# Kernel optimization log

Measured on AMD Instinct MI355X. Metric: run time of the kernel, lower is better.

The kernel has to match this reference:

```python
import jax, jax.numpy as jnp
import numpy as np

D_MODEL = 1024
NUM_HEADS = 16
D_K = D_MODEL // NUM_HEADS


def setup_inputs() -> dict:
    key = jax.random.key(0)
    ks = jax.random.split(key, 12)
    B, S = 2, 2048
    s = 1.0 / np.sqrt(D_MODEL)
    inp = {
        "query": jax.random.normal(ks[0], (B, S, D_MODEL), jnp.float32),
        "key": jax.random.normal(ks[1], (B, S, D_MODEL), jnp.float32),
        "value": jax.random.normal(ks[2], (B, S, D_MODEL), jnp.float32),
        "Wq": jax.random.normal(ks[3], (D_MODEL, D_MODEL), jnp.float32) * s,
        "bq": jax.random.normal(ks[4], (D_MODEL,), jnp.float32) * s,
        "Wk": jax.random.normal(ks[5], (D_MODEL, D_MODEL), jnp.float32) * s,
        "bk": jax.random.normal(ks[6], (D_MODEL,), jnp.float32) * s,
        "Wv": jax.random.normal(ks[7], (D_MODEL, D_MODEL), jnp.float32) * s,
        "bv": jax.random.normal(ks[8], (D_MODEL,), jnp.float32) * s,
        "Wo": jax.random.normal(ks[9], (D_MODEL, D_MODEL), jnp.float32) * s,
        "bo": jax.random.normal(ks[10], (D_MODEL,), jnp.float32) * s,
    }
    return inp


def _split_heads(x):
    B, S, _ = x.shape
    return x.reshape(B, S, NUM_HEADS, D_K).transpose(0, 2, 1, 3)  # [B,H,S,Dk]


def reference(query, key, value, Wq, bq, Wk, bk, Wv, bv, Wo, bo):
    # Linear projections (torch Linear: x @ W.T + b)
    Q = _split_heads(query @ Wq.T + bq)
    K = _split_heads(key @ Wk.T + bk)
    V = _split_heads(value @ Wv.T + bv)
    scale = 1.0 / jnp.sqrt(jnp.asarray(D_K, Q.dtype))
    scores = jnp.einsum('bhqd,bhkd->bhqk', Q, K) * scale  # [B,H,S,S]
    attn = jax.nn.softmax(scores, axis=-1)
    # dropout is identity in eval mode
    x = jnp.einsum('bhqk,bhkd->bhqd', attn, V)
    B, H, S, Dk = x.shape
    x = x.transpose(0, 2, 1, 3).reshape(B, S, H * Dk)
    return x @ Wo.T + bo
```

## Files before the change

kernel.cpp:

```cpp
#include <hip/hip_runtime.h>
#include <hip/hip_bf16.h>

typedef __bf16 bf16;
typedef __attribute__((ext_vector_type(4))) __bf16 bf16x4;
typedef __attribute__((ext_vector_type(8))) __bf16 bf16x8;
typedef __attribute__((ext_vector_type(4))) float f32x4;
typedef __attribute__((ext_vector_type(16))) float f32x16;
typedef unsigned int u32;

#define D_MODEL 1024
#define NHEADS 16
#define DK 64
#define BATCH 2
#define SEQ 2048
#define NTOK (BATCH * SEQ)

#define QSCALE 0.18033688011112042f
#define DEFER_THR 8.0f

__device__ __forceinline__ u32 cvtpk_bf16(float lo, float hi) {
  u32 r;
  asm("v_cvt_pk_bf16_f32 %0, %1, %2" : "=v"(r) : "v"(lo), "v"(hi));
  return r;
}
__device__ __forceinline__ void plswap(u32& a, u32& b) {
  asm("v_permlane32_swap_b32 %0, %1" : "+v"(a), "+v"(b));
}
__device__ __forceinline__ float fast_exp2(float x) {
#if __has_builtin(__builtin_amdgcn_exp2f)
  return __builtin_amdgcn_exp2f(x);
#else
  return exp2f(x);
#endif
}
__device__ __forceinline__ float xhalf_max(float x) {
  return fmaxf(x, __shfl_xor(x, 32));
}
__device__ __forceinline__ float xhalf_add(float x) {
  return x + __shfl_xor(x, 32);
}

__device__ __forceinline__ int frag_off_q(int s, int d) {
  return ((s >> 5) << 11) + ((d >> 4) << 9) + ((((d >> 3) & 1) * 32 + (s & 31)) << 3) + (d & 7);
}
__device__ __forceinline__ int frag_off_k(int s, int d) {
  return ((s >> 6) << 12) + ((((s >> 5) & 1) * 4 + (d >> 4)) << 9) +
         ((((d >> 3) & 1) * 32 + (s & 31)) << 3) + (d & 7);
}
__device__ __forceinline__ int frag_off_v(int s, int d) {
  return ((s >> 6) << 12) + (((d >> 5) * 4 + ((s >> 4) & 3)) << 9) +
         ((((s >> 3) & 1) * 32 + (d & 31)) << 3) + (s & 7);
}

__global__ __launch_bounds__(256) void cvt3_kernel(
    const float* __restrict__ s0, const float* __restrict__ s1, const float* __restrict__ s2,
    bf16* __restrict__ d0, bf16* __restrict__ d1, bf16* __restrict__ d2, int n4) {
  int i = blockIdx.x * blockDim.x + threadIdx.x;
  if (i >= n4) return;
  const float* s = blockIdx.y == 0 ? s0 : blockIdx.y == 1 ? s1 : s2;
  bf16* d = blockIdx.y == 0 ? d0 : blockIdx.y == 1 ? d1 : d2;
  float4 v = reinterpret_cast<const float4*>(s)[i];
  bf16x4 o;
  o[0] = (bf16)v.x; o[1] = (bf16)v.y; o[2] = (bf16)v.z; o[3] = (bf16)v.w;
  reinterpret_cast<bf16x4*>(d)[i] = o;
}

__global__ __launch_bounds__(256) void cvt4_kernel(
    const float* __restrict__ s0, const float* __restrict__ s1,
    const float* __restrict__ s2, const float* __restrict__ s3,
    bf16* __restrict__ d0, bf16* __restrict__ d1, bf16* __restrict__ d2, bf16* __restrict__ d3,
    int n4) {
  int i = blockIdx.x * blockDim.x + threadIdx.x;
  if (i >= n4) return;
  const float* s = blockIdx.y == 0 ? s0 : blockIdx.y == 1 ? s1 : blockIdx.y == 2 ? s2 : s3;
  bf16* d = blockIdx.y == 0 ? d0 : blockIdx.y == 1 ? d1 : blockIdx.y == 2 ? d2 : d3;
  float4 v = reinterpret_cast<const float4*>(s)[i];
  bf16x4 o;
  o[0] = (bf16)v.x; o[1] = (bf16)v.y; o[2] = (bf16)v.z; o[3] = (bf16)v.w;
  reinterpret_cast<bf16x4*>(d)[i] = o;
}

#define ASYNC_COPY16(gptr, lptr)                                                \
  __builtin_amdgcn_global_load_lds(                                             \
      (__attribute__((address_space(1))) void*)(gptr),                          \
      (__attribute__((address_space(3))) void*)(lptr), 16, 0, 0)

struct ProjArgs {
  const bf16* A[3];
  const bf16* W[3];
  const float* bias[3];
  bf16* out[3];
};

__global__ __launch_bounds__(256) void gemm_proj(ProjArgs pa, int K) {
  __shared__ bf16 As[128][32];
  __shared__ bf16 Bs[128][32];
  const int z = blockIdx.z;
  const bf16* A = pa.A[z];
  const bf16* Bw = pa.W[z];
  const int m0 = blockIdx.x * 128;
  const int n0 = blockIdx.y * 128;

  const int t = threadIdx.x;
  const int wave = t >> 6;
  const int lane = t & 63;
  const int wr = (wave >> 1) * 64;
  const int wc = (wave & 1) * 64;
  const int r4 = lane >> 2;
  const int c8 = (lane & 3) * 8;
  const int fr = lane & 15;
  const int fk = (lane >> 4) * 8;

  f32x4 acc[4][4] = {};

  for (int k0 = 0; k0 < K; k0 += 32) {
    ASYNC_COPY16(&A[(size_t)(m0 + wave * 16 + r4) * K + k0 + c8], &As[wave * 16][0]);
    ASYNC_COPY16(&A[(size_t)(m0 + 64 + wave * 16 + r4) * K + k0 + c8], &As[64 + wave * 16][0]);
    ASYNC_COPY16(&Bw[(size_t)(n0 + wave * 16 + r4) * K + k0 + c8], &Bs[wave * 16][0]);
    ASYNC_COPY16(&Bw[(size_t)(n0 + 64 + wave * 16 + r4) * K + k0 + c8], &Bs[64 + wave * 16][0]);
    __syncthreads();

    bf16x8 af[4], bfr[4];
#pragma unroll
    for (int m = 0; m < 4; m++)
      af[m] = *reinterpret_cast<const bf16x8*>(&As[wr + m * 16 + fr][fk]);
#pragma unroll
    for (int n = 0; n < 4; n++)
      bfr[n] = *reinterpret_cast<const bf16x8*>(&Bs[wc + n * 16 + fr][fk]);
#pragma unroll
    for (int m = 0; m < 4; m++)
#pragma unroll
      for (int n = 0; n < 4; n++)
        acc[m][n] = __builtin_amdgcn_mfma_f32_16x16x32_bf16(af[m], bfr[n], acc[m][n], 0, 0, 0);
    __syncthreads();
  }

  const float scale = (z == 0) ? QSCALE : 1.0f;
  const float* bias = pa.bias[z];
  bf16* out = pa.out[z];
#pragma unroll
  for (int m = 0; m < 4; m++) {
#pragma unroll
    for (int n = 0; n < 4; n++) {
      const int col = n0 + wc + n * 16 + fr;
      const float bv = bias[col];
#pragma unroll
      for (int j = 0; j < 4; j++) {
        const int row = m0 + wr + m * 16 + (lane >> 4) * 4 + j;
        const float v = (acc[m][n][j] + bv) * scale;
        const int b = row >> 11;
        const int s = row & (SEQ - 1);
        const int h = col >> 6;
        const int d = col & (DK - 1);
        const size_t base = (size_t)(b * NHEADS + h) * SEQ * DK;
        int off;
        if (z == 0)      off = frag_off_q(s, d);
        else if (z == 1) off = frag_off_k(s, d);
        else             off = frag_off_v(s, d);
        out[base + off] = (bf16)v;
      }
    }
  }
}

#define TM 128
#define TN 64
#define BK 32

__global__ __launch_bounds__(256) void gemm_out(
    const bf16* __restrict__ A, const bf16* __restrict__ Bw,
    const float* __restrict__ bias, float* __restrict__ out, int K) {
  __shared__ bf16 As[TM][BK];
  __shared__ bf16 Bs[TN][BK];
  const int m0 = blockIdx.x * TM;
  const int n0 = blockIdx.y * TN;

  const int t = threadIdx.x;
  const int wave = t >> 6;
  const int lane = t & 63;
  const int wr = (wave >> 1) * 64;
  const int wc = (wave & 1) * 32;
  const int r4 = lane >> 2;
  const int c8 = (lane & 3) * 8;
  const int fr = lane & 15;
  const int fk = (lane >> 4) * 8;

  f32x4 acc[4][2] = {};
  for (int k0 = 0; k0 < K; k0 += BK) {
    ASYNC_COPY16(&A[(size_t)(m0 + wave * 16 + r4) * K + k0 + c8], &As[wave * 16][0]);
    ASYNC_COPY16(&A[(size_t)(m0 + 64 + wave * 16 + r4) * K + k0 + c8], &As[64 + wave * 16][0]);
    ASYNC_COPY16(&Bw[(size_t)(n0 + wave * 16 + r4) * K + k0 + c8], &Bs[wave * 16][0]);
    __syncthreads();

    bf16x8 af[4], bfr[2];
#pragma unroll
    for (int m = 0; m < 4; m++)
      af[m] = *reinterpret_cast<const bf16x8*>(&As[wr + m * 16 + fr][fk]);
#pragma unroll
    for (int n = 0; n < 2; n++)
      bfr[n] = *reinterpret_cast<const bf16x8*>(&Bs[wc + n * 16 + fr][fk]);
#pragma unroll
    for (int m = 0; m < 4; m++)
#pragma unroll
      for (int n = 0; n < 2; n++)
        acc[m][n] = __builtin_amdgcn_mfma_f32_16x16x32_bf16(af[m], bfr[n], acc[m][n], 0, 0, 0);
    __syncthreads();
  }

#pragma unroll
  for (int m = 0; m < 4; m++) {
#pragma unroll
    for (int n = 0; n < 2; n++) {
      const int col = n0 + wc + n * 16 + fr;
      const float bv = bias[col];
#pragma unroll
      for (int j = 0; j < 4; j++) {
        const int row = m0 + wr + m * 16 + (lane >> 4) * 4 + j;
        out[(size_t)row * D_MODEL + col] = acc[m][n][j] + bv;
      }
    }
  }
}

#define QBLK 32
#define KVBLK 64
#define NT (SEQ / KVBLK)
#define NLOC (NT / 2)

__global__ __launch_bounds__(128, 2) void attn_kernel(
    const bf16* __restrict__ Qf,
    const bf16* __restrict__ Kf,
    const bf16* __restrict__ Vf,
    bf16* __restrict__ X) {
  __shared__ float lds_o[32][64];
  __shared__ float lds_ml[2][64];

  const int lane = threadIdx.x & 63;
  const int wave = threadIdx.x >> 6;
  const int bh = blockIdx.y;
  const int bb = bh >> 4, hh = bh & (NHEADS - 1);
  const int q0 = blockIdx.x * QBLK;
  const int row = lane & 31, hi = lane >> 5;

  const bf16* Qp = Qf + (size_t)bh * SEQ * DK + (size_t)q0 * DK;
  const bf16* Kp = Kf + (size_t)bh * SEQ * DK;
  const bf16* Vp = Vf + (size_t)bh * SEQ * DK;

  bf16x8 qf[4];
#pragma unroll
  for (int kd = 0; kd < 4; kd++)
    qf[kd] = *reinterpret_cast<const bf16x8*>(&Qp[kd * 512 + lane * 8]);

  f32x16 ot0, ot1;
#pragma unroll
  for (int r = 0; r < 16; r++) { ot0[r] = 0.f; ot1[r] = 0.f; }
  float m_run = -1e30f, l_run = 0.f;

  bf16x8 ka[2][4], kb2[2][4];

#define LOADK(dst, tt)                                                          \
  {                                                                             \
    const bf16* kbase_ = Kp + (size_t)(tt) * 4096 + lane * 8;                   \
    _Pragma("unroll") for (int hf = 0; hf < 2; hf++)                            \
        _Pragma("unroll") for (int kd = 0; kd < 4; kd++)                        \
            dst[hf][kd] = *reinterpret_cast<const bf16x8*>(                     \
                &kbase_[(hf * 4 + kd) * 512]);                                  \
  }

  auto gt = [&](int i) { return wave + 2 * (i & (NLOC - 1)); };

  LOADK(ka, gt(0))
  LOADK(kb2, gt(1))
  f32x16 sa0, sa1, sb0, sb1;
#pragma unroll
  for (int r = 0; r < 16; r++) { sa0[r] = 0.f; sa1[r] = 0.f; }
  __builtin_amdgcn_s_setprio(1);
#pragma unroll
  for (int kd = 0; kd < 4; kd++)
    sa0 = __builtin_amdgcn_mfma_f32_32x32x16_bf16(ka[0][kd], qf[kd], sa0, 0, 0, 0);
#pragma unroll
  for (int kd = 0; kd < 4; kd++)
    sa1 = __builtin_amdgcn_mfma_f32_32x32x16_bf16(ka[1][kd], qf[kd], sa1, 0, 0, 0);
  __builtin_amdgcn_s_setprio(0);

  auto pipe = [&](f32x16& SC0, f32x16& SC1, f32x16& SN0, f32x16& SN1,
                  bf16x8 (&KN)[2][4], bf16x8 (&KL)[2][4], int tc, int tp) {
#pragma unroll
    for (int r = 0; r < 16; r++) { SN0[r] = 0.f; SN1[r] = 0.f; }
    __builtin_amdgcn_s_setprio(1);
#pragma unroll
    for (int kd = 0; kd < 4; kd++)
      SN0 = __builtin_amdgcn_mfma_f32_32x32x16_bf16(KN[0][kd], qf[kd], SN0, 0, 0, 0);
#pragma unroll
    for (int kd = 0; kd < 4; kd++)
      SN1 = __builtin_amdgcn_mfma_f32_32x32x16_bf16(KN[1][kd], qf[kd], SN1, 0, 0, 0);
    __builtin_amdgcn_s_setprio(0);

    LOADK(KL, tp)

    bf16x8 vf[2][4];
    {
      const bf16* vbase_ = Vp + (size_t)tc * 4096 + lane * 8;
#pragma unroll
      for (int dh = 0; dh < 2; dh++)
#pragma unroll
        for (int ks = 0; ks < 4; ks++)
          vf[dh][ks] = *reinterpret_cast<const bf16x8*>(&vbase_[(dh * 4 + ks) * 512]);
    }

    float w16[16];
#pragma unroll
    for (int r = 0; r < 16; r++) w16[r] = fmaxf(SC0[r], SC1[r]);
#pragma unroll
    for (int r = 0; r < 8; r++) w16[r] = fmaxf(w16[r], w16[r + 8]);
#pragma unroll
    for (int r = 0; r < 4; r++) w16[r] = fmaxf(w16[r], w16[r + 4]);
    float mx = fmaxf(fmaxf(w16[0], w16[1]), fmaxf(w16[2], w16[3]));
    mx = xhalf_max(mx);
    if (__any(mx > m_run + DEFER_THR)) {
      const float mn = fmaxf(m_run, mx);
      const float alpha = fast_exp2(m_run - mn);
      m_run = mn;
      l_run *= alpha;
#pragma unroll
      for (int r = 0; r < 16; r++) { ot0[r] *= alpha; ot1[r] *= alpha; }
    }
    float p[32];
#pragma unroll
    for (int r = 0; r < 16; r++) p[r] = fast_exp2(SC0[r] - m_run);
#pragma unroll
    for (int r = 0; r < 16; r++) p[16 + r] = fast_exp2(SC1[r] - m_run);
    float a16[16];
#pragma unroll
    for (int r = 0; r < 16; r++) a16[r] = p[r] + p[r + 16];
#pragma unroll
    for (int r = 0; r < 8; r++) a16[r] += a16[r + 8];
#pragma unroll
    for (int r = 0; r < 4; r++) a16[r] += a16[r + 4];
    float rs = (a16[0] + a16[1]) + (a16[2] + a16[3]);
    l_run += xhalf_add(rs);

    u32 c[16];
#pragma unroll
    for (int i = 0; i < 8; i++) c[i] = cvtpk_bf16(p[2 * i], p[2 * i + 1]);
#pragma unroll
    for (int i = 0; i < 8; i++) c[8 + i] = cvtpk_bf16(p[16 + 2 * i], p[17 + 2 * i]);
    plswap(c[0], c[2]);   plswap(c[1], c[3]);
    plswap(c[4], c[6]);   plswap(c[5], c[7]);
    plswap(c[8], c[10]);  plswap(c[9], c[11]);
    plswap(c[12], c[14]); plswap(c[13], c[15]);
    bf16x8 pbv[4];
#pragma unroll
    for (int ks = 0; ks < 4; ks++) {
      union { u32 u[4]; bf16x8 v; } pk;
      pk.u[0] = c[ks * 4 + 0]; pk.u[1] = c[ks * 4 + 1];
      pk.u[2] = c[ks * 4 + 2]; pk.u[3] = c[ks * 4 + 3];
      pbv[ks] = pk.v;
    }

    __builtin_amdgcn_s_setprio(1);
#pragma unroll
    for (int ks = 0; ks < 4; ks++) {
      ot0 = __builtin_amdgcn_mfma_f32_32x32x16_bf16(vf[0][ks], pbv[ks], ot0, 0, 0, 0);
      ot1 = __builtin_amdgcn_mfma_f32_32x32x16_bf16(vf[1][ks], pbv[ks], ot1, 0, 0, 0);
    }
    __builtin_amdgcn_s_setprio(0);
  };

  for (int i = 0; i < NLOC; i += 2) {
    pipe(sa0, sa1, sb0, sb1, kb2, ka, gt(i), gt(i + 2));
    pipe(sb0, sb1, sa0, sa1, ka, kb2, gt(i + 1), gt(i + 3));
  }

  if (wave == 1) {
#pragma unroll
    for (int r = 0; r < 16; r++) {
      lds_o[r][lane] = ot0[r];
      lds_o[16 + r][lane] = ot1[r];
    }
    lds_ml[0][lane] = m_run;
    lds_ml[1][lane] = l_run;
  }
  __syncthreads();
  if (wave == 0) {
    const float m1 = lds_ml[0][lane];
    const float l1 = lds_ml[1][lane];
    const float mm = fmaxf(m_run, m1);
    const float s0 = fast_exp2(m_run - mm);
    const float s1 = fast_exp2(m1 - mm);
    const float inv = 1.0f / (l_run * s0 + l1 * s1);
    bf16* Xp = X + ((size_t)bb * SEQ + q0 + row) * D_MODEL + hh * DK;
#pragma unroll
    for (int g = 0; g < 4; g++) {
      bf16x4 w0, w1;
#pragma unroll
      for (int j = 0; j < 4; j++) {
        w0[j] = (bf16)((ot0[g * 4 + j] * s0 + lds_o[g * 4 + j][lane] * s1) * inv);
        w1[j] = (bf16)((ot1[g * 4 + j] * s0 + lds_o[16 + g * 4 + j][lane] * s1) * inv);
      }
      *reinterpret_cast<bf16x4*>(&Xp[g * 8 + hi * 4]) = w0;
      *reinterpret_cast<bf16x4*>(&Xp[32 + g * 8 + hi * 4]) = w1;
    }
  }
}

extern "C" void kernel_launch(void* const* d_in, const int* in_sizes, int n_in,
                              void* d_out, int out_size, void* d_ws, size_t ws_size,
                              hipStream_t stream) {
  const float* q  = (const float*)d_in[0];
  const float* k  = (const float*)d_in[1];
  const float* v  = (const float*)d_in[2];
  const float* Wq = (const float*)d_in[3];
  const float* bq = (const float*)d_in[4];
  const float* Wk = (const float*)d_in[5];
  const float* bk = (const float*)d_in[6];
  const float* Wv = (const float*)d_in[7];
  const float* bv = (const float*)d_in[8];
  const float* Wo = (const float*)d_in[9];
  const float* bo = (const float*)d_in[10];

  char* ws = (char*)d_ws;
  size_t off = 0;
  auto alloc = [&](size_t bytes) -> void* {
    void* p = ws + off;
    off += (bytes + 255) & ~(size_t)255;
    return p;
  };
  const size_t ACT = (size_t)NTOK * D_MODEL;
  const size_t WEL = (size_t)D_MODEL * D_MODEL;

  bf16* Xq  = (bf16*)alloc(ACT * 2);
  bf16* Xk  = (bf16*)alloc(ACT * 2);
  bf16* Xv  = (bf16*)alloc(ACT * 2);
  bf16* Wqb = (bf16*)alloc(WEL * 2);
  bf16* Wkb = (bf16*)alloc(WEL * 2);
  bf16* Wvb = (bf16*)alloc(WEL * 2);
  bf16* Wob = (bf16*)alloc(WEL * 2);
  bf16* Qfb = (bf16*)alloc(ACT * 2);
  bf16* Kfb = (bf16*)alloc(ACT * 2);
  bf16* Vfb = (bf16*)alloc(ACT * 2);
  bf16* Xa  = (bf16*)alloc(ACT * 2);

  {
    int n4 = (int)(ACT / 4);
    cvt3_kernel<<<dim3((n4 + 255) / 256, 3), dim3(256), 0, stream>>>(q, k, v, Xq, Xk, Xv, n4);
  }
  {
    int n4 = (int)(WEL / 4);
    cvt4_kernel<<<dim3((n4 + 255) / 256, 4), dim3(256), 0, stream>>>(
        Wq, Wk, Wv, Wo, Wqb, Wkb, Wvb, Wob, n4);
  }

  ProjArgs pa;
  pa.A[0] = Xq;  pa.A[1] = Xk;  pa.A[2] = Xv;
  pa.W[0] = Wqb; pa.W[1] = Wkb; pa.W[2] = Wvb;
  pa.bias[0] = bq; pa.bias[1] = bk; pa.bias[2] = bv;
  pa.out[0] = Qfb; pa.out[1] = Kfb; pa.out[2] = Vfb;
  gemm_proj<<<dim3(NTOK / 128, D_MODEL / 128, 3), dim3(256), 0, stream>>>(pa, D_MODEL);

  attn_kernel<<<dim3(SEQ / QBLK, BATCH * NHEADS), dim3(128), 0, stream>>>(
      Qfb, Kfb, Vfb, Xa);

  gemm_out<<<dim3(NTOK / TM, D_MODEL / TN), dim3(256), 0, stream>>>(
      Xa, Wob, bo, (float*)d_out, D_MODEL);
}
```

Measured before the change: 143.4 us.

## Drop intra-block KV split; each wave owns full KV range, XCD-aware head mapping

Before, two waves split the KV sequence of one 32-row query tile and merged partial softmax state through LDS. Now each of four waves per block handles its own 32-query tile over the whole KV range, so the LDS merge and the barrier go away. The grid becomes 1D with 512 blocks, and block indices are remapped so all blocks of one head land on the same XCD, keeping K/V reuse in that XCD's L2. The cost is a serial KV loop per wave that is twice as long, so per-wave latency rises, with parallelism coming only from more waves per block.

```diff
diff --git a/kernel.cpp b/kernel.cpp
--- a/kernel.cpp
+++ b/kernel.cpp
@@ -225,21 +225,23 @@
 #define QBLK 32
 #define KVBLK 64
 #define NT (SEQ / KVBLK)
-#define NLOC (NT / 2)
-
-__global__ __launch_bounds__(128, 2) void attn_kernel(
+
+__global__ __launch_bounds__(256, 2) void attn_kernel(
     const bf16* __restrict__ Qf,
     const bf16* __restrict__ Kf,
     const bf16* __restrict__ Vf,
     bf16* __restrict__ X) {
-  __shared__ float lds_o[32][64];
-  __shared__ float lds_ml[2][64];
-
   const int lane = threadIdx.x & 63;
   const int wave = threadIdx.x >> 6;
-  const int bh = blockIdx.y;
+
+  const int i = blockIdx.x;
+  const int xcd = i & 7;
+  const int slot = i >> 3;
+  const int hgrp = slot >> 4;
+  const int xq = slot & 15;
+  const int bh = xcd + 8 * hgrp;
   const int bb = bh >> 4, hh = bh & (NHEADS - 1);
-  const int q0 = blockIdx.x * QBLK;
+  const int q0 = xq * (QBLK * 4) + wave * QBLK;
   const int row = lane & 31, hi = lane >> 5;
 
   const bf16* Qp = Qf + (size_t)bh * SEQ * DK + (size_t)q0 * DK;
@@ -267,10 +269,8 @@
                 &kbase_[(hf * 4 + kd) * 512]);                                  \
   }
 
-  auto gt = [&](int i) { return wave + 2 * (i & (NLOC - 1)); };
-
-  LOADK(ka, gt(0))
-  LOADK(kb2, gt(1))
+  LOADK(ka, 0)
+  LOADK(kb2, 1)
   f32x16 sa0, sa1, sb0, sb1;
 #pragma unroll
   for (int r = 0; r < 16; r++) { sa0[r] = 0.f; sa1[r] = 0.f; }
@@ -284,7 +284,7 @@
   __builtin_amdgcn_s_setprio(0);
 
   auto pipe = [&](f32x16& SC0, f32x16& SC1, f32x16& SN0, f32x16& SN1,
-                  bf16x8 (&KN)[2][4], bf16x8 (&KL)[2][4], int tc, int tp) {
+                  bf16x8 (&KN)[2][4], bf16x8 (&KL)[2][4], int tc) {
 #pragma unroll
     for (int r = 0; r < 16; r++) { SN0[r] = 0.f; SN1[r] = 0.f; }
     __builtin_amdgcn_s_setprio(1);
@@ -296,7 +296,7 @@
       SN1 = __builtin_amdgcn_mfma_f32_32x32x16_bf16(KN[1][kd], qf[kd], SN1, 0, 0, 0);
     __builtin_amdgcn_s_setprio(0);
 
-    LOADK(KL, tp)
+    LOADK(KL, (tc + 2) & (NT - 1))
 
     bf16x8 vf[2][4];
     {
@@ -342,9 +342,9 @@
 
     u32 c[16];
 #pragma unroll
-    for (int i = 0; i < 8; i++) c[i] = cvtpk_bf16(p[2 * i], p[2 * i + 1]);
-#pragma unroll
-    for (int i = 0; i < 8; i++) c[8 + i] = cvtpk_bf16(p[16 + 2 * i], p[17 + 2 * i]);
+    for (int i2 = 0; i2 < 8; i2++) c[i2] = cvtpk_bf16(p[2 * i2], p[2 * i2 + 1]);
+#pragma unroll
+    for (int i2 = 0; i2 < 8; i2++) c[8 + i2] = cvtpk_bf16(p[16 + 2 * i2], p[17 + 2 * i2]);
     plswap(c[0], c[2]);   plswap(c[1], c[3]);
     plswap(c[4], c[6]);   plswap(c[5], c[7]);
     plswap(c[8], c[10]);  plswap(c[9], c[11]);
@@ -367,40 +367,23 @@
     __builtin_amdgcn_s_setprio(0);
   };
 
-  for (int i = 0; i < NLOC; i += 2) {
-    pipe(sa0, sa1, sb0, sb1, kb2, ka, gt(i), gt(i + 2));
-    pipe(sb0, sb1, sa0, sa1, ka, kb2, gt(i + 1), gt(i + 3));
-  }
-
-  if (wave == 1) {
-#pragma unroll
-    for (int r = 0; r < 16; r++) {
-      lds_o[r][lane] = ot0[r];
-      lds_o[16 + r][lane] = ot1[r];
-    }
-    lds_ml[0][lane] = m_run;
-    lds_ml[1][lane] = l_run;
-  }
-  __syncthreads();
-  if (wave == 0) {
-    const float m1 = lds_ml[0][lane];
-    const float l1 = lds_ml[1][lane];
-    const float mm = fmaxf(m_run, m1);
-    const float s0 = fast_exp2(m_run - mm);
-    const float s1 = fast_exp2(m1 - mm);
-    const float inv = 1.0f / (l_run * s0 + l1 * s1);
-    bf16* Xp = X + ((size_t)bb * SEQ + q0 + row) * D_MODEL + hh * DK;
-#pragma unroll
-    for (int g = 0; g < 4; g++) {
-      bf16x4 w0, w1;
-#pragma unroll
-      for (int j = 0; j < 4; j++) {
-        w0[j] = (bf16)((ot0[g * 4 + j] * s0 + lds_o[g * 4 + j][lane] * s1) * inv);
-        w1[j] = (bf16)((ot1[g * 4 + j] * s0 + lds_o[16 + g * 4 + j][lane] * s1) * inv);
-      }
-      *reinterpret_cast<bf16x4*>(&Xp[g * 8 + hi * 4]) = w0;
-      *reinterpret_cast<bf16x4*>(&Xp[32 + g * 8 + hi * 4]) = w1;
-    }
+  for (int t = 0; t < NT; t += 2) {
+    pipe(sa0, sa1, sb0, sb1, kb2, ka, t);
+    pipe(sb0, sb1, sa0, sa1, ka, kb2, t + 1);
+  }
+
+  const float inv = 1.0f / l_run;
+  bf16* Xp = X + ((size_t)bb * SEQ + q0 + row) * D_MODEL + hh * DK;
+#pragma unroll
+  for (int g = 0; g < 4; g++) {
+    bf16x4 w0, w1;
+#pragma unroll
+    for (int j = 0; j < 4; j++) {
+      w0[j] = (bf16)(ot0[g * 4 + j] * inv);
+      w1[j] = (bf16)(ot1[g * 4 + j] * inv);
+    }
+    *reinterpret_cast<bf16x4*>(&Xp[g * 8 + hi * 4]) = w0;
+    *reinterpret_cast<bf16x4*>(&Xp[32 + g * 8 + hi * 4]) = w1;
   }
 }
 
@@ -458,8 +441,7 @@
   pa.out[0] = Qfb; pa.out[1] = Kfb; pa.out[2] = Vfb;
   gemm_proj<<<dim3(NTOK / 128, D_MODEL / 128, 3), dim3(256), 0, stream>>>(pa, D_MODEL);
 
-  attn_kernel<<<dim3(SEQ / QBLK, BATCH * NHEADS), dim3(128), 0, stream>>>(
-      Qfb, Kfb, Vfb, Xa);
+  attn_kernel<<<dim3(512), dim3(256), 0, stream>>>(Qfb, Kfb, Vfb, Xa);
 
   gemm_out<<<dim3(NTOK / TM, D_MODEL / TN), dim3(256), 0, stream>>>(
       Xa, Wob, bo, (float*)d_out, D_MODEL);
```

Measured after the change: 136.9 us. 4.6% less time.
